# Kernel tuning notes

Hardware: AMD Instinct MI355X
Metric: run time of the kernel (lower is better)

Reference implementation:

```python
import jax, jax.numpy as jnp
import numpy as np

N_EMBD = 1024
N_HEAD = 16
HEAD = N_EMBD // N_HEAD
B, T = 4, 2048


def setup_inputs() -> dict:
    key = jax.random.key(0)
    ks = jax.random.split(key, 9)
    s = 1.0 / np.sqrt(N_EMBD)
    return {
        "x": jax.random.normal(ks[0], (B, T, N_EMBD), dtype=jnp.float32),
        "Wk": jax.random.uniform(ks[1], (N_EMBD, N_EMBD), jnp.float32, -s, s),
        "bk": jax.random.uniform(ks[2], (N_EMBD,), jnp.float32, -s, s),
        "Wq": jax.random.uniform(ks[3], (N_EMBD, N_EMBD), jnp.float32, -s, s),
        "bq": jax.random.uniform(ks[4], (N_EMBD,), jnp.float32, -s, s),
        "Wv": jax.random.uniform(ks[5], (N_EMBD, N_EMBD), jnp.float32, -s, s),
        "bv": jax.random.uniform(ks[6], (N_EMBD,), jnp.float32, -s, s),
        "Wp": jax.random.uniform(ks[7], (N_EMBD, N_EMBD), jnp.float32, -s, s),
        "bp": jax.random.uniform(ks[8], (N_EMBD,), jnp.float32, -s, s),
    }


def reference(x, Wk, bk, Wq, bq, Wv, bv, Wp, bp):
    b, t, c = x.shape
    # torch Linear: y = x @ W.T + b
    def heads(W, bias):
        return (x @ W.T + bias).reshape(b, t, N_HEAD, HEAD).transpose(0, 2, 1, 3)
    k = heads(Wk, bk)  # [B,H,T,D]
    q = heads(Wq, bq)
    v = heads(Wv, bv)
    att = jnp.einsum("bhqd,bhkd->bhqk", q, k) * (1.0 / np.sqrt(HEAD))
    causal = jnp.tril(jnp.ones((t, t), dtype=bool))
    att = jnp.where(causal, att, -jnp.inf)
    att = jax.nn.softmax(att, axis=-1)
    y = jnp.einsum("bhqk,bhkd->bhqd", att, v)  # [B,H,T,D]
    y = y.transpose(0, 2, 1, 3).reshape(b, t, c)
    return y @ Wp.T + bp
```

## Files before the change

kernel.cpp:

```cpp
#include <hip/hip_runtime.h>
#include <stdint.h>

typedef short bf16x8 __attribute__((ext_vector_type(8)));
typedef float f32x4 __attribute__((ext_vector_type(4)));
typedef float f32x16 __attribute__((ext_vector_type(16)));

#define MFMA16(a, b, c) __builtin_amdgcn_mfma_f32_16x16x32_bf16((a), (b), (c), 0, 0, 0)
#define MFMA32(a, b, c) __builtin_amdgcn_mfma_f32_32x32x16_bf16((a), (b), (c), 0, 0, 0)

__device__ __forceinline__ unsigned short f2bf(float x) {
  union { float f; unsigned int u; } v; v.f = x;
  unsigned int r = (v.u + 0x7FFFu + ((v.u >> 16) & 1u)) >> 16;
  return (unsigned short)r;
}

__device__ __forceinline__ unsigned int cvtpk(float lo, float hi) {
  unsigned int r;
  asm("v_cvt_pk_bf16_f32 %0, %1, %2" : "=v"(r) : "v"(lo), "v"(hi));
  return r;
}

__device__ __forceinline__ void plswap(unsigned int& a, unsigned int& b) {
  asm("v_permlane32_swap_b32 %0, %1" : "+v"(a), "+v"(b));
}

__device__ __forceinline__ float exp2f_fast(float x) {
  float r;
  asm("v_exp_f32 %0, %1" : "=v"(r) : "v"(x));
  return r;
}

__global__ void __launch_bounds__(256) cvt_all(const float* __restrict__ x,
                                               const float* __restrict__ Wk,
                                               const float* __restrict__ Wq,
                                               const float* __restrict__ Wv,
                                               const float* __restrict__ Wp,
                                               unsigned short* __restrict__ xb,
                                               unsigned short* __restrict__ wqkvb,
                                               unsigned short* __restrict__ wpb) {
  const int stride = gridDim.x * blockDim.x;
  for (int i = blockIdx.x * blockDim.x + threadIdx.x; i < 3145728; i += stride) {
    const float4* s4;
    ushort4* d4;
    int off;
    if (i < 2097152) {
      s4 = (const float4*)x; d4 = (ushort4*)xb; off = i;
      float4 v = s4[off];
      ushort4 o;
      o.x = f2bf(v.x); o.y = f2bf(v.y); o.z = f2bf(v.z); o.w = f2bf(v.w);
      d4[i < 2097152 ? i : 0] = o;
      ((ushort4*)xb)[i] = o;
      continue;
    }
    int j = i - 2097152;
    int sec = j >> 18;
    off = j & 262143;
    s4 = (const float4*)(sec == 0 ? Wk : sec == 1 ? Wq : sec == 2 ? Wv : Wp);
    float4 v = s4[off];
    ushort4 o;
    o.x = f2bf(v.x); o.y = f2bf(v.y); o.z = f2bf(v.z); o.w = f2bf(v.w);
    if (sec < 3) ((ushort4*)wqkvb)[j] = o;
    else ((ushort4*)wpb)[off] = o;
  }
}

template <int MODE, int NX, int CPX>
__global__ void __launch_bounds__(512) gemm_big(const unsigned short* __restrict__ A,
                                                const unsigned short* __restrict__ Bw,
                                                const float* __restrict__ b0,
                                                const float* __restrict__ b1,
                                                const float* __restrict__ b2,
                                                unsigned short* __restrict__ O0,
                                                unsigned short* __restrict__ O1,
                                                unsigned short* __restrict__ O2,
                                                float* __restrict__ Of) {
  extern __shared__ unsigned short lds[];

  const int tid = threadIdx.x;
  const int wid = tid >> 6;
  const int l = tid & 63;
  const int g = l >> 4;
  const int ln = l & 15;

  const int bid = blockIdx.x;
  const int swz = (bid & 7) * CPX + (bid >> 3);
  const int bx = swz % NX;
  const int by = swz / NX;
  const int m0 = by * 256;
  const int n0 = bx * 128;
  const int wm = (wid >> 1) * 64;
  const int wn = (wid & 1) * 64;

  f32x4 acc[4][4];
#pragma unroll
  for (int i = 0; i < 4; ++i)
#pragma unroll
    for (int j = 0; j < 4; ++j) acc[i][j] = (f32x4){0.f, 0.f, 0.f, 0.f};

#define STAGE_G(bufi, kt)                                                                         \
  {                                                                                               \
    unsigned short* Ad = lds + (bufi)*16384;                                                      \
    unsigned short* Bd = lds + 32768 + (bufi)*8192;                                               \
    _Pragma("unroll") for (int i = 0; i < 4; ++i) {                                               \
      int c = i * 512 + tid;                                                                      \
      int row = c >> 3;                                                                           \
      int cs = (c & 7) ^ (row & 7);                                                               \
      const unsigned short* ga = A + (size_t)(m0 + row) * 1024 + (kt) + cs * 8;                   \
      __builtin_amdgcn_global_load_lds((const __attribute__((address_space(1))) void*)ga,         \
                                       (__attribute__((address_space(3))) void*)&Ad[c * 8],       \
                                       16, 0, 0);                                                 \
    }                                                                                             \
    _Pragma("unroll") for (int i = 0; i < 2; ++i) {                                               \
      int c = i * 512 + tid;                                                                      \
      int row = c >> 3;                                                                           \
      int cs = (c & 7) ^ (row & 7);                                                               \
      const unsigned short* gb = Bw + (size_t)(n0 + row) * 1024 + (kt) + cs * 8;                  \
      __builtin_amdgcn_global_load_lds((const __attribute__((address_space(1))) void*)gb,         \
                                       (__attribute__((address_space(3))) void*)&Bd[c * 8],       \
                                       16, 0, 0);                                                 \
    }                                                                                             \
  }

  STAGE_G(0, 0);
  __syncthreads();

  for (int T = 0; T < 16; ++T) {
    const int buf = T & 1;
    if (T < 15) STAGE_G(buf ^ 1, (T + 1) * 64);

    const unsigned short* Ar = lds + buf * 16384;
    const unsigned short* Br = lds + 32768 + buf * 8192;
#pragma unroll
    for (int kk = 0; kk < 2; ++kk) {
      bf16x8 af[4], bfr[4];
#pragma unroll
      for (int mi = 0; mi < 4; ++mi) {
        int ra = wm + mi * 16 + ln;
        af[mi] = *(const bf16x8*)&Ar[ra * 64 + (((kk << 2) + g) ^ (ra & 7)) * 8];
      }
#pragma unroll
      for (int ni = 0; ni < 4; ++ni) {
        int rb = wn + ni * 16 + ln;
        bfr[ni] = *(const bf16x8*)&Br[rb * 64 + (((kk << 2) + g) ^ (rb & 7)) * 8];
      }
      __builtin_amdgcn_s_setprio(1);
#pragma unroll
      for (int mi = 0; mi < 4; ++mi)
#pragma unroll
        for (int ni = 0; ni < 4; ++ni) acc[mi][ni] = MFMA16(af[mi], bfr[ni], acc[mi][ni]);
      __builtin_amdgcn_s_setprio(0);
    }
    __syncthreads();
  }
#undef STAGE_G

  const int mBase = m0 + wm + g * 4;
  const int nBase = n0 + wn + ln;

  if (MODE == 1) {
#pragma unroll
    for (int mi = 0; mi < 4; ++mi) {
      int mg = mBase + mi * 16;
#pragma unroll
      for (int ni = 0; ni < 4; ++ni) {
        int n = nBase + ni * 16;
        float bvl = b0[n];
#pragma unroll
        for (int r = 0; r < 4; ++r) Of[(size_t)(mg + r) * 1024 + n] = acc[mi][ni][r] + bvl;
      }
    }
  } else {
    const int sec = n0 >> 10;
    const float* bias = (sec == 0) ? b0 : (sec == 1) ? b1 : b2;
#pragma unroll
    for (int mi = 0; mi < 4; ++mi) {
      int mg = mBase + mi * 16;
      int b = mg >> 11, t = mg & 2047;
#pragma unroll
      for (int ni = 0; ni < 4; ++ni) {
        int n = nBase + ni * 16;
        int nn = n & 1023;
        int h = nn >> 6, d = nn & 63;
        float bvl = bias[nn];
        if (sec == 2) {
          ushort4 pk;
          pk.x = f2bf(acc[mi][ni][0] + bvl);
          pk.y = f2bf(acc[mi][ni][1] + bvl);
          pk.z = f2bf(acc[mi][ni][2] + bvl);
          pk.w = f2bf(acc[mi][ni][3] + bvl);
          *(ushort4*)&O2[((size_t)((b * 16 + h) * 64 + d)) * 2048 + t] = pk;
        } else {
          unsigned short* O = sec ? O1 : O0;
          const float sc = sec ? (0.125f * 1.44269504f) : 1.0f;
#pragma unroll
          for (int r = 0; r < 4; ++r)
            O[((size_t)(b * 16 + h) * 2048 + (t + r)) * 64 + d] = f2bf((acc[mi][ni][r] + bvl) * sc);
        }
      }
    }
  }
}

__global__ void __launch_bounds__(512) attn_kernel(const unsigned short* __restrict__ Q,
                                                   const unsigned short* __restrict__ K,
                                                   const unsigned short* __restrict__ Vt,
                                                   unsigned short* __restrict__ Y) {
  __shared__ unsigned short Ks[2][64 * 64];
  __shared__ unsigned short Vs[2][64 * 64];

  const int tid = threadIdx.x;
  const int wid = tid >> 6;
  const int l = tid & 63;
  const int q32 = l & 31;
  const int hi = l >> 5;
  const int bh = blockIdx.x & 63;
  const int hb = blockIdx.x >> 6;
  const int sb = (hb < 4) ? (7 - hb) : (hb - 4);
  const int q0w = sb * 256 + wid * 32;
  const int NT = 4 * sb + 4;
  const int myNt = (q0w + 95) >> 6;

  const unsigned short* Qp = Q + (size_t)bh * 2048 * 64;
  const unsigned short* Kp = K + (size_t)bh * 2048 * 64;
  const unsigned short* Vp = Vt + (size_t)bh * 64 * 2048;
  const int b = bh >> 4, h = bh & 15;

  const int srow = tid >> 3;
  const int csw = (tid & 7) ^ (srow & 7);

  bf16x8 qf[4];
#pragma unroll
  for (int kk = 0; kk < 4; ++kk)
    qf[kk] = *(const bf16x8*)&Qp[(size_t)(q0w + q32) * 64 + kk * 16 + hi * 8];

  f32x16 o0, o1;
#pragma unroll
  for (int r = 0; r < 16; ++r) { o0[r] = 0.f; o1[r] = 0.f; }
  float m = -1e30f, lst = 0.f;

#define STAGE(bufi, kk0)                                                                        \
  {                                                                                             \
    const unsigned short* gk = Kp + (size_t)((kk0) + srow) * 64 + csw * 8;                      \
    const unsigned short* gv = Vp + (size_t)srow * 2048 + (kk0) + csw * 8;                      \
    __builtin_amdgcn_global_load_lds((const __attribute__((address_space(1))) void*)gk,         \
                                     (__attribute__((address_space(3))) void*)                  \
                                         &Ks[bufi][wid * 512],                                  \
                                     16, 0, 0);                                                 \
    __builtin_amdgcn_global_load_lds((const __attribute__((address_space(1))) void*)gv,         \
                                     (__attribute__((address_space(3))) void*)                  \
                                         &Vs[bufi][wid * 512],                                  \
                                     16, 0, 0);                                                 \
  }

  int buf = 0;
  STAGE(0, 0);
  __syncthreads();

  for (int t = 0; t < NT; ++t) {
    const int k0 = t * 64;
    if (t + 1 < NT) STAGE(buf ^ 1, k0 + 64);

    if (t < myNt) {
      const int xr = q32 & 7;
      f32x16 s0, s1;
#pragma unroll
      for (int r = 0; r < 16; ++r) { s0[r] = 0.f; s1[r] = 0.f; }
      __builtin_amdgcn_s_setprio(1);
#pragma unroll
      for (int kk = 0; kk < 4; ++kk) {
        bf16x8 kf0 = *(const bf16x8*)&Ks[buf][q32 * 64 + (((kk << 1) | hi) ^ xr) * 8];
        bf16x8 kf1 = *(const bf16x8*)&Ks[buf][(32 + q32) * 64 + (((kk << 1) | hi) ^ xr) * 8];
        s0 = MFMA32(kf0, qf[kk], s0);
        s1 = MFMA32(kf1, qf[kk], s1);
      }
      __builtin_amdgcn_s_setprio(0);

      if (k0 + 63 > q0w) {
        const int qg = q0w + q32;
#pragma unroll
        for (int r = 0; r < 16; ++r) {
          int kr = (r & 3) + 8 * (r >> 2) + 4 * hi;
          if (k0 + kr > qg) s0[r] = -1e30f;
          if (k0 + 32 + kr > qg) s1[r] = -1e30f;
        }
      }

      float pm = fmaxf(fmaxf(s0[0], s0[1]), s0[2]);
#pragma unroll
      for (int r = 3; r < 15; r += 3) pm = fmaxf(fmaxf(fmaxf(s0[r], s0[r + 1]), s0[r + 2]), pm);
      pm = fmaxf(pm, s0[15]);
#pragma unroll
      for (int r = 0; r < 15; r += 3) pm = fmaxf(fmaxf(fmaxf(s1[r], s1[r + 1]), s1[r + 2]), pm);
      pm = fmaxf(pm, s1[15]);
      pm = fmaxf(pm, __shfl_xor(pm, 32));

      if (__any(pm > m + 11.0f)) {
        float mn = fmaxf(m, pm);
        float sf = exp2f_fast(m - mn);
        m = mn;
        lst *= sf;
#pragma unroll
        for (int r = 0; r < 16; ++r) {
          float sb2 = __shfl(sf, (r & 3) + 8 * (r >> 2) + 4 * hi);
          o0[r] *= sb2;
          o1[r] *= sb2;
        }
      }
      float rs = 0.f;
#pragma unroll
      for (int r = 0; r < 16; ++r) { s0[r] = exp2f_fast(s0[r] - m); rs += s0[r]; }
#pragma unroll
      for (int r = 0; r < 16; ++r) { s1[r] = exp2f_fast(s1[r] - m); rs += s1[r]; }
      rs += __shfl_xor(rs, 32);
      lst += rs;

      union { unsigned int u[4]; bf16x8 v; } pa[4];
#pragma unroll
      for (int t2 = 0; t2 < 2; ++t2) {
        const f32x16& sv = t2 ? s1 : s0;
#pragma unroll
        for (int sl = 0; sl < 2; ++sl) {
          int base = sl * 8;
          unsigned int x0 = cvtpk(sv[base + 0], sv[base + 1]);
          unsigned int x1 = cvtpk(sv[base + 2], sv[base + 3]);
          unsigned int x2 = cvtpk(sv[base + 4], sv[base + 5]);
          unsigned int x3 = cvtpk(sv[base + 6], sv[base + 7]);
          plswap(x0, x2);
          plswap(x1, x3);
          int ksg = t2 * 2 + sl;
          pa[ksg].u[0] = x0; pa[ksg].u[1] = x1; pa[ksg].u[2] = x2; pa[ksg].u[3] = x3;
        }
      }

      __builtin_amdgcn_s_setprio(1);
#pragma unroll
      for (int ksg = 0; ksg < 4; ++ksg) {
        bf16x8 v0 = *(const bf16x8*)&Vs[buf][q32 * 64 + (((ksg << 1) | hi) ^ xr) * 8];
        bf16x8 v1 = *(const bf16x8*)&Vs[buf][(32 + q32) * 64 + (((ksg << 1) | hi) ^ xr) * 8];
        o0 = MFMA32(pa[ksg].v, v0, o0);
        o1 = MFMA32(pa[ksg].v, v1, o1);
      }
      __builtin_amdgcn_s_setprio(0);
    }

    __syncthreads();
    buf ^= 1;
  }

#pragma unroll
  for (int r = 0; r < 16; ++r) {
    int qsrc = (r & 3) + 8 * (r >> 2) + 4 * hi;
    int qg = q0w + qsrc;
    float lq = __shfl(lst, qsrc);
    float inv = 1.0f / lq;
    size_t rowb = (size_t)(b * 2048 + qg) * 1024 + h * 64;
    Y[rowb + q32] = f2bf(o0[r] * inv);
    Y[rowb + 32 + q32] = f2bf(o1[r] * inv);
  }
#undef STAGE
}

extern "C" void kernel_launch(void* const* d_in, const int* in_sizes, int n_in,
                              void* d_out, int out_size, void* d_ws, size_t ws_size,
                              hipStream_t stream) {
  const float* x = (const float*)d_in[0];
  const float* Wk = (const float*)d_in[1];
  const float* bk = (const float*)d_in[2];
  const float* Wq = (const float*)d_in[3];
  const float* bq = (const float*)d_in[4];
  const float* Wv = (const float*)d_in[5];
  const float* bv = (const float*)d_in[6];
  const float* Wp = (const float*)d_in[7];
  const float* bp = (const float*)d_in[8];
  float* out = (float*)d_out;

  char* ws = (char*)d_ws;
  unsigned short* xb    = (unsigned short*)(ws);
  unsigned short* wqkvb = (unsigned short*)(ws + 16777216);
  unsigned short* wpb   = (unsigned short*)(ws + 23068672);
  unsigned short* Qb    = (unsigned short*)(ws + 25165824);
  unsigned short* Kb    = (unsigned short*)(ws + 41943040);
  unsigned short* Vtb   = (unsigned short*)(ws + 58720256);
  unsigned short* yb    = (unsigned short*)(ws + 75497472);
  if (ws_size < 92274688u) return;

  const int LDS_BYTES = 98304;
  (void)hipFuncSetAttribute((const void*)&gemm_big<0, 24, 96>,
                            hipFuncAttributeMaxDynamicSharedMemorySize, LDS_BYTES);
  (void)hipFuncSetAttribute((const void*)&gemm_big<1, 8, 32>,
                            hipFuncAttributeMaxDynamicSharedMemorySize, LDS_BYTES);

  cvt_all<<<dim3(3072), dim3(256), 0, stream>>>(x, Wk, Wq, Wv, Wp, xb, wqkvb, wpb);

  gemm_big<0, 24, 96><<<dim3(768), dim3(512), LDS_BYTES, stream>>>(
      xb, wqkvb, bk, bq, bv, Kb, Qb, Vtb, nullptr);

  attn_kernel<<<dim3(512), dim3(512), 0, stream>>>(Qb, Kb, Vtb, yb);

  gemm_big<1, 8, 32><<<dim3(256), dim3(512), LDS_BYTES, stream>>>(
      yb, wpb, bp, nullptr, nullptr, nullptr, nullptr, nullptr, out);
}
```

Before: 155.2 us.

## Single-buffer GEMM LDS and split attention into smaller 128-row query blocks

The GEMM drops its double-buffered LDS pipeline in favour of a single buffer with two barriers per k-tile, which halves dynamic LDS to 48KB so more workgroups can be resident per CU. The attention kernel moves from 512-thread blocks covering 256 query rows to 256-thread blocks covering 128 rows, with a constant permutation table that interleaves long and short causal blocks. The aim is better occupancy and load balance, at the cost of losing global-to-LDS overlap inside each GEMM workgroup. The conversion kernel also loses a redundant duplicate store.

New measurement: 182.4 us. +17.6%, slower.

```diff
diff --git a/kernel.cpp b/kernel.cpp
--- a/kernel.cpp
+++ b/kernel.cpp
@@ -40,22 +40,17 @@
                                                unsigned short* __restrict__ wpb) {
   const int stride = gridDim.x * blockDim.x;
   for (int i = blockIdx.x * blockDim.x + threadIdx.x; i < 3145728; i += stride) {
-    const float4* s4;
-    ushort4* d4;
-    int off;
     if (i < 2097152) {
-      s4 = (const float4*)x; d4 = (ushort4*)xb; off = i;
-      float4 v = s4[off];
+      float4 v = ((const float4*)x)[i];
       ushort4 o;
       o.x = f2bf(v.x); o.y = f2bf(v.y); o.z = f2bf(v.z); o.w = f2bf(v.w);
-      d4[i < 2097152 ? i : 0] = o;
       ((ushort4*)xb)[i] = o;
       continue;
     }
     int j = i - 2097152;
     int sec = j >> 18;
-    off = j & 262143;
-    s4 = (const float4*)(sec == 0 ? Wk : sec == 1 ? Wq : sec == 2 ? Wv : Wp);
+    int off = j & 262143;
+    const float4* s4 = (const float4*)(sec == 0 ? Wk : sec == 1 ? Wq : sec == 2 ? Wv : Wp);
     float4 v = s4[off];
     ushort4 o;
     o.x = f2bf(v.x); o.y = f2bf(v.y); o.z = f2bf(v.z); o.w = f2bf(v.w);
@@ -97,17 +92,15 @@
 #pragma unroll
     for (int j = 0; j < 4; ++j) acc[i][j] = (f32x4){0.f, 0.f, 0.f, 0.f};
 
-#define STAGE_G(bufi, kt)                                                                         \
+#define STAGE_G(kt)                                                                               \
   {                                                                                               \
-    unsigned short* Ad = lds + (bufi)*16384;                                                      \
-    unsigned short* Bd = lds + 32768 + (bufi)*8192;                                               \
     _Pragma("unroll") for (int i = 0; i < 4; ++i) {                                               \
       int c = i * 512 + tid;                                                                      \
       int row = c >> 3;                                                                           \
       int cs = (c & 7) ^ (row & 7);                                                               \
       const unsigned short* ga = A + (size_t)(m0 + row) * 1024 + (kt) + cs * 8;                   \
       __builtin_amdgcn_global_load_lds((const __attribute__((address_space(1))) void*)ga,         \
-                                       (__attribute__((address_space(3))) void*)&Ad[c * 8],       \
+                                       (__attribute__((address_space(3))) void*)&lds[c * 8],      \
                                        16, 0, 0);                                                 \
     }                                                                                             \
     _Pragma("unroll") for (int i = 0; i < 2; ++i) {                                               \
@@ -116,20 +109,19 @@
       int cs = (c & 7) ^ (row & 7);                                                               \
       const unsigned short* gb = Bw + (size_t)(n0 + row) * 1024 + (kt) + cs * 8;                  \
       __builtin_amdgcn_global_load_lds((const __attribute__((address_space(1))) void*)gb,         \
-                                       (__attribute__((address_space(3))) void*)&Bd[c * 8],       \
+                                       (__attribute__((address_space(3))) void*)                  \
+                                           &lds[16384 + c * 8],                                   \
                                        16, 0, 0);                                                 \
     }                                                                                             \
   }
 
-  STAGE_G(0, 0);
-  __syncthreads();
-
   for (int T = 0; T < 16; ++T) {
-    const int buf = T & 1;
-    if (T < 15) STAGE_G(buf ^ 1, (T + 1) * 64);
-
-    const unsigned short* Ar = lds + buf * 16384;
-    const unsigned short* Br = lds + 32768 + buf * 8192;
+    __syncthreads();
+    STAGE_G(T * 64);
+    __syncthreads();
+
+    const unsigned short* Ar = lds;
+    const unsigned short* Br = lds + 16384;
 #pragma unroll
     for (int kk = 0; kk < 2; ++kk) {
       bf16x8 af[4], bfr[4];
@@ -150,7 +142,6 @@
         for (int ni = 0; ni < 4; ++ni) acc[mi][ni] = MFMA16(af[mi], bfr[ni], acc[mi][ni]);
       __builtin_amdgcn_s_setprio(0);
     }
-    __syncthreads();
   }
 #undef STAGE_G
 
@@ -201,7 +192,7 @@
   }
 }
 
-__global__ void __launch_bounds__(512) attn_kernel(const unsigned short* __restrict__ Q,
+__global__ void __launch_bounds__(256) attn_kernel(const unsigned short* __restrict__ Q,
                                                    const unsigned short* __restrict__ K,
                                                    const unsigned short* __restrict__ Vt,
                                                    unsigned short* __restrict__ Y) {
@@ -214,10 +205,12 @@
   const int q32 = l & 31;
   const int hi = l >> 5;
   const int bh = blockIdx.x & 63;
-  const int hb = blockIdx.x >> 6;
-  const int sb = (hb < 4) ? (7 - hb) : (hb - 4);
-  const int q0w = sb * 256 + wid * 32;
-  const int NT = 4 * sb + 4;
+  const int u = blockIdx.x >> 6;
+  __constant__ static const int perm[16] = {15, 13, 11, 9, 0, 2, 4, 6,
+                                            14, 12, 10, 8, 1, 3, 5, 7};
+  const int qblk = perm[u];
+  const int q0w = qblk * 128 + wid * 32;
+  const int NT = 2 * qblk + 2;
   const int myNt = (q0w + 95) >> 6;
 
   const unsigned short* Qp = Q + (size_t)bh * 2048 * 64;
@@ -225,9 +218,6 @@
   const unsigned short* Vp = Vt + (size_t)bh * 64 * 2048;
   const int b = bh >> 4, h = bh & 15;
 
-  const int srow = tid >> 3;
-  const int csw = (tid & 7) ^ (srow & 7);
-
   bf16x8 qf[4];
 #pragma unroll
   for (int kk = 0; kk < 4; ++kk)
@@ -240,16 +230,21 @@
 
 #define STAGE(bufi, kk0)                                                                        \
   {                                                                                             \
-    const unsigned short* gk = Kp + (size_t)((kk0) + srow) * 64 + csw * 8;                      \
-    const unsigned short* gv = Vp + (size_t)srow * 2048 + (kk0) + csw * 8;                      \
-    __builtin_amdgcn_global_load_lds((const __attribute__((address_space(1))) void*)gk,         \
-                                     (__attribute__((address_space(3))) void*)                  \
-                                         &Ks[bufi][wid * 512],                                  \
-                                     16, 0, 0);                                                 \
-    __builtin_amdgcn_global_load_lds((const __attribute__((address_space(1))) void*)gv,         \
-                                     (__attribute__((address_space(3))) void*)                  \
-                                         &Vs[bufi][wid * 512],                                  \
-                                     16, 0, 0);                                                 \
+    _Pragma("unroll") for (int i = 0; i < 2; ++i) {                                             \
+      int c = i * 256 + tid;                                                                    \
+      int row = c >> 3;                                                                         \
+      int csw = (c & 7) ^ (row & 7);                                                            \
+      const unsigned short* gk = Kp + (size_t)((kk0) + row) * 64 + csw * 8;                     \
+      const unsigned short* gv = Vp + (size_t)row * 2048 + (kk0) + csw * 8;                     \
+      __builtin_amdgcn_global_load_lds((const __attribute__((address_space(1))) void*)gk,       \
+                                       (__attribute__((address_space(3))) void*)                \
+                                           &Ks[bufi][c * 8],                                    \
+                                       16, 0, 0);                                               \
+      __builtin_amdgcn_global_load_lds((const __attribute__((address_space(1))) void*)gv,       \
+                                       (__attribute__((address_space(3))) void*)                \
+                                           &Vs[bufi][c * 8],                                    \
+                                       16, 0, 0);                                               \
+    }                                                                                           \
   }
 
   int buf = 0;
@@ -384,7 +379,7 @@
   unsigned short* yb    = (unsigned short*)(ws + 75497472);
   if (ws_size < 92274688u) return;
 
-  const int LDS_BYTES = 98304;
+  const int LDS_BYTES = 49152;
   (void)hipFuncSetAttribute((const void*)&gemm_big<0, 24, 96>,
                             hipFuncAttributeMaxDynamicSharedMemorySize, LDS_BYTES);
   (void)hipFuncSetAttribute((const void*)&gemm_big<1, 8, 32>,
@@ -395,7 +390,7 @@
   gemm_big<0, 24, 96><<<dim3(768), dim3(512), LDS_BYTES, stream>>>(
       xb, wqkvb, bk, bq, bv, Kb, Qb, Vtb, nullptr);
 
-  attn_kernel<<<dim3(512), dim3(512), 0, stream>>>(Qb, Kb, Vtb, yb);
+  attn_kernel<<<dim3(1024), dim3(256), 0, stream>>>(Qb, Kb, Vtb, yb);
 
   gemm_big<1, 8, 32><<<dim3(256), dim3(512), LDS_BYTES, stream>>>(
       yb, wpb, bp, nullptr, nullptr, nullptr, nullptr, nullptr, out);
```
